# Performance work log

Hardware: AMD Instinct MI355X
Metric: run time of the kernel (lower is better)

## Reference

```python
import jax, jax.numpy as jnp
import numpy as np

N, E, D_IN, D_H, D_OUT = 100000, 1600000, 128, 128, 16


def setup_inputs() -> dict:
    key = jax.random.key(0)
    k_x, k_e, k_w1, k_w2 = jax.random.split(key, 4)
    x = jax.random.normal(k_x, (N, D_IN), dtype=jnp.float32)
    edge_index = jax.random.randint(k_e, (2, E), 0, N, dtype=jnp.int64)
    # glorot-ish init for the two GCNConv weight matrices
    W1 = jax.random.normal(k_w1, (D_IN, D_H), dtype=jnp.float32) * (1.0 / np.sqrt(D_IN))
    b1 = jnp.zeros((D_H,), dtype=jnp.float32)
    W2 = jax.random.normal(k_w2, (D_H, D_OUT), dtype=jnp.float32) * (1.0 / np.sqrt(D_H))
    b2 = jnp.zeros((D_OUT,), dtype=jnp.float32)
    return {"x": x, "edge_index": edge_index, "W1": W1, "b1": b1, "W2": W2, "b2": b2}


def _gcn_conv(x, src, dst, norm, W, b, n):
    # linear transform, gather from source nodes, normalize, scatter-add to targets
    h = x @ W                                   # [N, d_out]
    msg = h[src] * norm[:, None]                # [E+N, d_out]
    return jax.ops.segment_sum(msg, dst, num_segments=n) + b


def reference(x, edge_index, W1, b1, W2, b2):
    n = x.shape[0]
    # GCNConv default: add self-loops, symmetric normalization D^-1/2 A D^-1/2
    loops = jnp.arange(n, dtype=edge_index.dtype)
    src = jnp.concatenate([edge_index[0], loops])
    dst = jnp.concatenate([edge_index[1], loops])
    deg = jax.ops.segment_sum(jnp.ones_like(dst, dtype=x.dtype), dst, num_segments=n)
    dinv = jnp.where(deg > 0, jax.lax.rsqrt(deg), 0.0)
    norm = dinv[src] * dinv[dst]                # [E+N]

    h = _gcn_conv(x, src, dst, norm, W1, b1, n)
    h = jax.nn.relu(h)
    # dropout is identity in eval mode (reference uses eval / deterministic path)
    out = _gcn_conv(h, src, dst, norm, W2, b2, n)
    return out
```

## Files before the change

### kernel.cpp

```cpp
#include <hip/hip_runtime.h>

typedef unsigned int uint;
typedef __attribute__((ext_vector_type(8))) short bf16x8;
typedef __attribute__((ext_vector_type(4))) float f32x4;

#define D_IN 128
#define D_H  128
#define D_OUT 16
#define NPC 512
#define NPCSH 9
#define CLDS 224
#define P1 256
#define XL_STRIDE 68
#define WT_STRIDE 68

static __device__ __forceinline__ float bflo(uint u) { return __uint_as_float(u << 16); }
static __device__ __forceinline__ float bfhi(uint u) { return __uint_as_float(u & 0xFFFF0000u); }
static __device__ __forceinline__ uint f2bf(float f) {
    uint b = __float_as_uint(f);
    return (b + 0x7FFFu + ((b >> 16) & 1u)) >> 16;
}
static __device__ __forceinline__ uint pk(float a, float b) {
    return f2bf(a) | (f2bf(b) << 16);
}


__global__ __launch_bounds__(256) void k_p1hist(const int* __restrict__ dst, int E, int N, int C,
                                                int chunk, int* __restrict__ hist1) {
    __shared__ int h[CLDS];
    int t = threadIdx.x, b = blockIdx.x;
    for (int i = t; i < C; i += 256) h[i] = 0;
    __syncthreads();
    int e0 = b * chunk, e1 = min(e0 + chunk, E);
    for (int e = e0 + t; e < e1; e += 256) {
        int d = dst[e];
        d = max(0, min(d, N - 1));
        atomicAdd(&h[d >> NPCSH], 1);
    }
    __syncthreads();
    for (int i = t; i < C; i += 256) hist1[(size_t)i * P1 + b] = h[i];
}

__global__ __launch_bounds__(1024) void k_p1scan(int* __restrict__ hist1, int C,
                                                 int* __restrict__ cbase) {
    __shared__ int col[CLDS];
    __shared__ int sdata[1024];
    int t = threadIdx.x;
    int w = t >> 6, lane = t & 63;
    for (int i = w; i < C; i += 16) {
        int4 v = ((const int4*)hist1)[i * 64 + lane];
        int s = v.x + v.y + v.z + v.w;
        int inc = s;
        for (int off = 1; off < 64; off <<= 1) {
            int o = __shfl_up(inc, off);
            if (lane >= off) inc += o;
        }
        int excl = inc - s;
        int4 p;
        p.x = excl;
        p.y = excl + v.x;
        p.z = excl + v.x + v.y;
        p.w = excl + v.x + v.y + v.z;
        ((int4*)hist1)[i * 64 + lane] = p;
        if (lane == 63) col[i] = inc;
    }
    __syncthreads();
    int v = (t < C) ? col[t] : 0;
    sdata[t] = v;
    __syncthreads();
    for (int off = 1; off < 1024; off <<= 1) {
        int x = (t >= off) ? sdata[t - off] : 0;
        __syncthreads();
        sdata[t] += x;
        __syncthreads();
    }
    int pos = sdata[t] - v;
    if (t < C) cbase[t] = pos;
    if (t == 1023) cbase[C] = sdata[1023];
    if (t < C) col[t] = pos;
    __syncthreads();
    for (int i = w; i < C; i += 16) {
        int base = col[i];
        int4 p = ((int4*)hist1)[i * 64 + lane];
        p.x += base; p.y += base; p.z += base; p.w += base;
        ((int4*)hist1)[i * 64 + lane] = p;
    }
}

__global__ __launch_bounds__(256) void k_p1fill(const int* __restrict__ src,
                                                const int* __restrict__ dst, int E, int N, int C,
                                                int chunk, const int* __restrict__ hist1,
                                                uint* __restrict__ binned1) {
    __shared__ int cur[CLDS];
    int t = threadIdx.x, b = blockIdx.x;
    for (int i = t; i < C; i += 256) cur[i] = hist1[(size_t)i * P1 + b];
    __syncthreads();
    int e0 = b * chunk, e1 = min(e0 + chunk, E);
    for (int e = e0 + t; e < e1; e += 256) {
        int d = dst[e];
        d = max(0, min(d, N - 1));
        int s = src[e];
        s = max(0, min(s, N - 1));
        int p = atomicAdd(&cur[d >> NPCSH], 1);
        binned1[p] = ((uint)(d & (NPC - 1)) << 17) | (uint)s;
    }
}

__global__ __launch_bounds__(256) void k_p2(const uint* __restrict__ binned1,
                                            const int* __restrict__ cbase, int N,
                                            int* __restrict__ ssrc, int* __restrict__ rowptr,
                                            int* __restrict__ deg, float* __restrict__ dinv) {
    __shared__ int ncnt[NPC], nbase_[NPC];
    __shared__ int sdata[256];
    int c = blockIdx.x, t = threadIdx.x;
    int start = cbase[c], end = cbase[c + 1];
    for (int i = t; i < NPC; i += 256) ncnt[i] = 0;
    __syncthreads();
    for (int j = start + t; j < end; j += 256) atomicAdd(&ncnt[binned1[j] >> 17], 1);
    __syncthreads();
    int v0 = ncnt[2 * t], v1 = ncnt[2 * t + 1];
    int s = v0 + v1;
    sdata[t] = s;
    __syncthreads();
    for (int off = 1; off < 256; off <<= 1) {
        int xv = (t >= off) ? sdata[t - off] : 0;
        __syncthreads();
        sdata[t] += xv;
        __syncthreads();
    }
    int pre = sdata[t] - s;
    nbase_[2 * t] = start + pre;
    nbase_[2 * t + 1] = start + pre + v0;
    __syncthreads();
    for (int i = t; i < NPC; i += 256) {
        int node = c * NPC + i;
        if (node < N) {
            deg[node] = ncnt[i];
            rowptr[node] = nbase_[i];
            dinv[node] = rsqrtf((float)ncnt[i] + 1.0f);
        }
    }
    __syncthreads();
    for (int i = t; i < NPC; i += 256) ncnt[i] = nbase_[i];
    __syncthreads();
    for (int j = start + t; j < end; j += 256) {
        uint pe = binned1[j];
        int p = atomicAdd(&ncnt[pe >> 17], 1);
        ssrc[p] = (int)(pe & 0x1FFFFu);
    }
}


__global__ __launch_bounds__(256) void k_packW1(const float* __restrict__ W1,
                                                uint* __restrict__ W1p) {
    int t = blockIdx.x * 256 + threadIdx.x;
    if (t >= 64 * 128) return;
    int k2 = t >> 7, f = t & 127;
    float w0 = W1[(size_t)(2 * k2) * 128 + f];
    float w1 = W1[(size_t)(2 * k2 + 1) * 128 + f];
    W1p[t] = pk(w0, w1);
}


__global__ __launch_bounds__(256) void k_gemm1(const uint* __restrict__ W1p,
                                               const float* __restrict__ x,
                                               const float* __restrict__ dinv, int N,
                                               uint* __restrict__ hs_b, int ntiles) {
    __shared__ uint Wt[128 * WT_STRIDE];
    __shared__ uint xl[64 * XL_STRIDE];
    int t = threadIdx.x;
    for (int p = t; p < 64 * 128; p += 256) {
        int k2 = p >> 7, f = p & 127;
        Wt[f * WT_STRIDE + k2] = W1p[p];
    }
    int w = t >> 6, lane = t & 63;
    int q = lane >> 4, m = lane & 15;
    const float4* x4 = (const float4*)x;
    for (int tile = blockIdx.x; tile < ntiles; tile += gridDim.x) {
        int row0 = tile * 64;
        __syncthreads();
        for (int p = t; p < 64 * 32; p += 256) {
            int r = p >> 5, c2 = p & 31;
            int gr = row0 + r;
            float4 v = (gr < N) ? x4[(size_t)gr * 32 + c2] : make_float4(0.f, 0.f, 0.f, 0.f);
            *(uint2*)&xl[r * XL_STRIDE + 2 * c2] = make_uint2(pk(v.x, v.y), pk(v.z, v.w));
        }
        __syncthreads();
        bf16x8 afr[4][4];
#pragma unroll
        for (int rt = 0; rt < 4; rt++)
#pragma unroll
            for (int kc = 0; kc < 4; kc++)
                afr[rt][kc] = *(const bf16x8*)&xl[(rt * 16 + m) * XL_STRIDE + kc * 16 + q * 4];
        f32x4 acc[2][4];
#pragma unroll
        for (int c = 0; c < 2; c++)
#pragma unroll
            for (int rt = 0; rt < 4; rt++) acc[c][rt] = (f32x4){0.f, 0.f, 0.f, 0.f};
#pragma unroll
        for (int c = 0; c < 2; c++) {
            int f = w * 32 + c * 16 + m;
#pragma unroll
            for (int kc = 0; kc < 4; kc++) {
                bf16x8 bfr = *(const bf16x8*)&Wt[f * WT_STRIDE + kc * 16 + q * 4];
#pragma unroll
                for (int rt = 0; rt < 4; rt++)
                    acc[c][rt] = __builtin_amdgcn_mfma_f32_16x16x32_bf16(afr[rt][kc], bfr,
                                                                         acc[c][rt], 0, 0, 0);
            }
        }
        __syncthreads();
        uint* outl = xl;
#pragma unroll
        for (int rt = 0; rt < 4; rt++) {
            int gb = row0 + rt * 16 + q * 4;
            float4 dv;
            if (gb + 3 < N) {
                dv = *(const float4*)&dinv[gb];
            } else {
                dv.x = (gb < N) ? dinv[gb] : 0.f;
                dv.y = (gb + 1 < N) ? dinv[gb + 1] : 0.f;
                dv.z = (gb + 2 < N) ? dinv[gb + 2] : 0.f;
                dv.w = (gb + 3 < N) ? dinv[gb + 3] : 0.f;
            }
            float dr[4] = {dv.x, dv.y, dv.z, dv.w};
#pragma unroll
            for (int c = 0; c < 2; c++) {
                f32x4 a = acc[c][rt];
#pragma unroll
                for (int r = 0; r < 4; r++) {
                    float v = a[r] * dr[r];
                    float vn = __shfl_xor(v, 1);
                    if (!(lane & 1)) {
                        int row = rt * 16 + q * 4 + r;
                        int cp = (w * 32 + c * 16 + m) >> 1;
                        outl[row * 65 + cp] = pk(v, vn);
                    }
                }
            }
        }
        __syncthreads();
        for (int p = t; p < 64 * 64; p += 256) {
            int r = p >> 6, cc = p & 63;
            int gr = row0 + r;
            if (gr < N) hs_b[(size_t)gr * 64 + cc] = outl[r * 65 + cc];
        }
    }
}


__global__ __launch_bounds__(256) void k_agg1(const uint* __restrict__ hs_b,
                                              const int* __restrict__ rowptr,
                                              const int* __restrict__ deg,
                                              const int* __restrict__ ssrc,
                                              const float* __restrict__ dinv,
                                              const float2* __restrict__ b1, int N,
                                              uint* __restrict__ rh_b) {
    int w = threadIdx.x >> 6, lane = threadIdx.x & 63;
    int d = blockIdx.x * 4 + w;
    if (d >= N) return;
    int start = rowptr[d], cnt = deg[d];
    uint sv = hs_b[(size_t)d * 64 + lane];
    float a0 = bflo(sv), a1 = bfhi(sv);
    int base = 0;
    while (base < cnt) {
        int nb = min(cnt - base, 64);
        int idxv = (lane < nb) ? ssrc[start + base + lane] : 0;
        int j = 0;
        for (; j + 16 <= nb; j += 16) {
            uint u[16];
#pragma unroll
            for (int q = 0; q < 16; q++) {
                int i = __shfl(idxv, j + q);
                u[q] = hs_b[(size_t)i * 64 + lane];
            }
#pragma unroll
            for (int q = 0; q < 16; q++) {
                a0 += bflo(u[q]);
                a1 += bfhi(u[q]);
            }
        }
        for (; j + 4 <= nb; j += 4) {
            uint u[4];
#pragma unroll
            for (int q = 0; q < 4; q++) {
                int i = __shfl(idxv, j + q);
                u[q] = hs_b[(size_t)i * 64 + lane];
            }
#pragma unroll
            for (int q = 0; q < 4; q++) {
                a0 += bflo(u[q]);
                a1 += bfhi(u[q]);
            }
        }
        for (; j < nb; j++) {
            int i = __shfl(idxv, j);
            uint u = hs_b[(size_t)i * 64 + lane];
            a0 += bflo(u);
            a1 += bfhi(u);
        }
        base += nb;
    }
    float sc = dinv[d];
    float2 bb = b1[lane];
    rh_b[(size_t)d * 64 + lane] =
        pk(fmaxf(fmaf(a0, sc, bb.x), 0.f), fmaxf(fmaf(a1, sc, bb.y), 0.f));
}


__global__ __launch_bounds__(256) void k_gemm2(const uint* __restrict__ rh_b,
                                               const float* __restrict__ W2,
                                               const float* __restrict__ dinv, int N,
                                               uint* __restrict__ h2_b) {
    __shared__ float Wl[D_H * D_OUT];
    int t = threadIdx.x;
    for (int i = t; i < D_H * D_OUT; i += 256) Wl[i] = W2[i];
    __syncthreads();
    int r = blockIdx.x * 256 + t;
    if (r >= N) return;
    const uint* xrow = rh_b + (size_t)r * 64;
    float acc[16];
#pragma unroll
    for (int f = 0; f < 16; f++) acc[f] = 0.f;
    for (int c = 0; c < 16; c++) {
        uint4 xv = *(const uint4*)(xrow + c * 4);
        uint xs[4] = {xv.x, xv.y, xv.z, xv.w};
#pragma unroll
        for (int u = 0; u < 4; u++) {
            int k = c * 8 + u * 2;
            float x0 = bflo(xs[u]), x1 = bfhi(xs[u]);
            const float* w0 = &Wl[k * 16];
            const float* w1 = &Wl[(k + 1) * 16];
#pragma unroll
            for (int f = 0; f < 16; f++) acc[f] = fmaf(x0, w0[f], acc[f]);
#pragma unroll
            for (int f = 0; f < 16; f++) acc[f] = fmaf(x1, w1[f], acc[f]);
        }
    }
    float sc = dinv[r];
    uint o[8];
#pragma unroll
    for (int q = 0; q < 8; q++) o[q] = pk(acc[2 * q] * sc, acc[2 * q + 1] * sc);
    *(uint4*)&h2_b[(size_t)r * 8] = make_uint4(o[0], o[1], o[2], o[3]);
    *(uint4*)&h2_b[(size_t)r * 8 + 4] = make_uint4(o[4], o[5], o[6], o[7]);
}


__global__ __launch_bounds__(256) void k_agg2(const uint* __restrict__ h2_b,
                                              const int* __restrict__ rowptr,
                                              const int* __restrict__ deg,
                                              const int* __restrict__ ssrc,
                                              const float* __restrict__ dinv,
                                              const float* __restrict__ b2, int N,
                                              float2* __restrict__ out) {
    int w = threadIdx.x >> 6, lane = threadIdx.x & 63;
    int d = blockIdx.x * 4 + w;
    if (d >= N) return;
    int slot = lane >> 3, jp = lane & 7;
    int start = rowptr[d], cnt = deg[d];
    float a0 = 0.f, a1 = 0.f;
    if (slot == 0) {
        uint sv = h2_b[(size_t)d * 8 + jp];
        a0 = bflo(sv);
        a1 = bfhi(sv);
    }
    int base = 0;
    while (base < cnt) {
        int nb = min(cnt - base, 64);
        int idxv = (lane < nb) ? ssrc[start + base + lane] : 0;
        int ngroups = (nb + 7) >> 3;
        for (int g = 0; g < ngroups; g++) {
            int j = g * 8 + slot;
            int i = __shfl(idxv, j);
            if (j < nb) {
                uint hv = h2_b[(size_t)i * 8 + jp];
                a0 += bflo(hv);
                a1 += bfhi(hv);
            }
        }
        base += nb;
    }
    a0 += __shfl_xor(a0, 8);
    a1 += __shfl_xor(a1, 8);
    a0 += __shfl_xor(a0, 16);
    a1 += __shfl_xor(a1, 16);
    a0 += __shfl_xor(a0, 32);
    a1 += __shfl_xor(a1, 32);
    if (slot == 0) {
        float di = dinv[d];
        out[(size_t)d * 8 + jp] =
            make_float2(fmaf(a0, di, b2[2 * jp]), fmaf(a1, di, b2[2 * jp + 1]));
    }
}


extern "C" void kernel_launch(void* const* d_in, const int* in_sizes, int n_in,
                              void* d_out, int out_size, void* d_ws, size_t ws_size,
                              hipStream_t stream) {
    const float* x  = (const float*)d_in[0];
    const int*   ei = (const int*)d_in[1];
    const float* W1 = (const float*)d_in[2];
    const float* b1 = (const float*)d_in[3];
    const float* W2 = (const float*)d_in[4];
    const float* b2 = (const float*)d_in[5];
    int N = in_sizes[0] / D_IN;
    int E = in_sizes[1] / 2;
    const int* src = ei;
    const int* dst = ei + E;
    int C = (N + NPC - 1) / NPC;
    int chunk = (E + P1 - 1) / P1;
    int ntiles = (N + 63) / 64;

    char* ws = (char*)d_ws;
    size_t off = 0;
    auto alloc = [&](size_t bytes) -> char* {
        char* p = ws + off;
        off = (off + bytes + 255) & ~(size_t)255;
        return p;
    };
    int*   hist1   = (int*)alloc((size_t)P1 * C * 4);
    int*   cbase   = (int*)alloc((size_t)(C + 1) * 4);
    uint*  binned1 = (uint*)alloc((size_t)E * 4);
    int*   ssrc    = (int*)alloc((size_t)E * 4);
    int*   rowptr  = (int*)alloc((size_t)N * 4);
    int*   deg     = (int*)alloc((size_t)N * 4);
    float* dinv    = (float*)alloc((size_t)N * 4);
    uint*  W1p     = (uint*)alloc((size_t)64 * 128 * 4);
    uint*  hs_b    = (uint*)alloc((size_t)N * 64 * 4);
    uint*  rh_b    = (uint*)alloc((size_t)N * 64 * 4);
    uint*  h2_b    = hs_b;

    k_packW1<<<32, 256, 0, stream>>>(W1, W1p);
    k_p1hist<<<P1, 256, 0, stream>>>(dst, E, N, C, chunk, hist1);
    k_p1scan<<<1, 1024, 0, stream>>>(hist1, C, cbase);
    k_p1fill<<<P1, 256, 0, stream>>>(src, dst, E, N, C, chunk, hist1, binned1);
    k_p2<<<C, 256, 0, stream>>>(binned1, cbase, N, ssrc, rowptr, deg, dinv);
    int g1 = min(768, ntiles);
    k_gemm1<<<g1, 256, 0, stream>>>(W1p, x, dinv, N, hs_b, ntiles);
    k_agg1<<<(N + 3) / 4, 256, 0, stream>>>(hs_b, rowptr, deg, ssrc, dinv,
                                            (const float2*)b1, N, rh_b);
    k_gemm2<<<(N + 255) / 256, 256, 0, stream>>>(rh_b, W2, dinv, N, h2_b);
    k_agg2<<<(N + 3) / 4, 256, 0, stream>>>(h2_b, rowptr, deg, ssrc, dinv, b2, N,
                                            (float2*)d_out);
}
```

Baseline: 295.1 us.

## Fuse CSR build with GEMM1, move source dinv scaling into aggregation

The W1 packing is folded into extra blocks of the histogram kernel, and the per-cluster CSR finalize (k_p2) now runs as extra blocks of the GEMM1 launch. GEMM1 no longer depends on dinv, so the two run concurrently. To allow this, the source-side dinv scaling moves from GEMM1's epilogue into agg1, which gathers dinv per neighbor and uses FMAs. agg2 also gets a specialized path for small-degree nodes that issues four independent loads per lane. The cost is two fewer launches and overlap of the CSR and GEMM work, traded for an extra random dinv gather per edge in agg1 and larger shared-memory use in the fused CSR blocks.

```diff
diff --git a/kernel.cpp b/kernel.cpp
--- a/kernel.cpp
+++ b/kernel.cpp
@@ -26,9 +26,19 @@
 
 
 __global__ __launch_bounds__(256) void k_p1hist(const int* __restrict__ dst, int E, int N, int C,
-                                                int chunk, int* __restrict__ hist1) {
+                                                int chunk, int* __restrict__ hist1,
+                                                const float* __restrict__ W1,
+                                                uint* __restrict__ W1p) {
     __shared__ int h[CLDS];
     int t = threadIdx.x, b = blockIdx.x;
+    if (b >= P1) {
+        int p = (b - P1) * 256 + t;
+        int k2 = p >> 7, f = p & 127;
+        float w0 = W1[(size_t)(2 * k2) * 128 + f];
+        float w1 = W1[(size_t)(2 * k2 + 1) * 128 + f];
+        W1p[p] = pk(w0, w1);
+        return;
+    }
     for (int i = t; i < C; i += 256) h[i] = 0;
     __syncthreads();
     int e0 = b * chunk, e1 = min(e0 + chunk, E);
@@ -106,69 +116,62 @@
     }
 }
 
-__global__ __launch_bounds__(256) void k_p2(const uint* __restrict__ binned1,
-                                            const int* __restrict__ cbase, int N,
-                                            int* __restrict__ ssrc, int* __restrict__ rowptr,
-                                            int* __restrict__ deg, float* __restrict__ dinv) {
-    __shared__ int ncnt[NPC], nbase_[NPC];
-    __shared__ int sdata[256];
-    int c = blockIdx.x, t = threadIdx.x;
-    int start = cbase[c], end = cbase[c + 1];
-    for (int i = t; i < NPC; i += 256) ncnt[i] = 0;
-    __syncthreads();
-    for (int j = start + t; j < end; j += 256) atomicAdd(&ncnt[binned1[j] >> 17], 1);
-    __syncthreads();
-    int v0 = ncnt[2 * t], v1 = ncnt[2 * t + 1];
-    int s = v0 + v1;
-    sdata[t] = s;
-    __syncthreads();
-    for (int off = 1; off < 256; off <<= 1) {
-        int xv = (t >= off) ? sdata[t - off] : 0;
-        __syncthreads();
-        sdata[t] += xv;
-        __syncthreads();
-    }
-    int pre = sdata[t] - s;
-    nbase_[2 * t] = start + pre;
-    nbase_[2 * t + 1] = start + pre + v0;
-    __syncthreads();
-    for (int i = t; i < NPC; i += 256) {
-        int node = c * NPC + i;
-        if (node < N) {
-            deg[node] = ncnt[i];
-            rowptr[node] = nbase_[i];
-            dinv[node] = rsqrtf((float)ncnt[i] + 1.0f);
-        }
-    }
-    __syncthreads();
-    for (int i = t; i < NPC; i += 256) ncnt[i] = nbase_[i];
-    __syncthreads();
-    for (int j = start + t; j < end; j += 256) {
-        uint pe = binned1[j];
-        int p = atomicAdd(&ncnt[pe >> 17], 1);
-        ssrc[p] = (int)(pe & 0x1FFFFu);
-    }
-}
-
-
-__global__ __launch_bounds__(256) void k_packW1(const float* __restrict__ W1,
-                                                uint* __restrict__ W1p) {
-    int t = blockIdx.x * 256 + threadIdx.x;
-    if (t >= 64 * 128) return;
-    int k2 = t >> 7, f = t & 127;
-    float w0 = W1[(size_t)(2 * k2) * 128 + f];
-    float w1 = W1[(size_t)(2 * k2 + 1) * 128 + f];
-    W1p[t] = pk(w0, w1);
-}
-
-
-__global__ __launch_bounds__(256) void k_gemm1(const uint* __restrict__ W1p,
-                                               const float* __restrict__ x,
-                                               const float* __restrict__ dinv, int N,
-                                               uint* __restrict__ hs_b, int ntiles) {
-    __shared__ uint Wt[128 * WT_STRIDE];
-    __shared__ uint xl[64 * XL_STRIDE];
+
+__global__ __launch_bounds__(256) void k_p2gemm1(const uint* __restrict__ binned1,
+                                                 const int* __restrict__ cbase, int N, int C,
+                                                 int* __restrict__ ssrc, int* __restrict__ rowptr,
+                                                 int* __restrict__ deg, float* __restrict__ dinv,
+                                                 const uint* __restrict__ W1p,
+                                                 const float* __restrict__ x,
+                                                 uint* __restrict__ hs_b, int ntiles) {
+    __shared__ uint smem[128 * WT_STRIDE + 64 * XL_STRIDE];
     int t = threadIdx.x;
+    if ((int)blockIdx.x < C) {
+        int* ncnt = (int*)smem;
+        int* nbase_ = ncnt + NPC;
+        int* sdata = nbase_ + NPC;
+        int c = blockIdx.x;
+        int start = cbase[c], end = cbase[c + 1];
+        for (int i = t; i < NPC; i += 256) ncnt[i] = 0;
+        __syncthreads();
+        for (int j = start + t; j < end; j += 256) atomicAdd(&ncnt[binned1[j] >> 17], 1);
+        __syncthreads();
+        int v0 = ncnt[2 * t], v1 = ncnt[2 * t + 1];
+        int s = v0 + v1;
+        sdata[t] = s;
+        __syncthreads();
+        for (int off = 1; off < 256; off <<= 1) {
+            int xv = (t >= off) ? sdata[t - off] : 0;
+            __syncthreads();
+            sdata[t] += xv;
+            __syncthreads();
+        }
+        int pre = sdata[t] - s;
+        nbase_[2 * t] = start + pre;
+        nbase_[2 * t + 1] = start + pre + v0;
+        __syncthreads();
+        for (int i = t; i < NPC; i += 256) {
+            int node = c * NPC + i;
+            if (node < N) {
+                deg[node] = ncnt[i];
+                rowptr[node] = nbase_[i];
+                dinv[node] = rsqrtf((float)ncnt[i] + 1.0f);
+            }
+        }
+        __syncthreads();
+        for (int i = t; i < NPC; i += 256) ncnt[i] = nbase_[i];
+        __syncthreads();
+        for (int j = start + t; j < end; j += 256) {
+            uint pe = binned1[j];
+            int p = atomicAdd(&ncnt[pe >> 17], 1);
+            ssrc[p] = (int)(pe & 0x1FFFFu);
+        }
+        return;
+    }
+    uint* Wt = smem;
+    uint* xl = smem + 128 * WT_STRIDE;
+    int role = blockIdx.x - C;
+    int nroles = gridDim.x - C;
     for (int p = t; p < 64 * 128; p += 256) {
         int k2 = p >> 7, f = p & 127;
         Wt[f * WT_STRIDE + k2] = W1p[p];
@@ -176,7 +179,7 @@
     int w = t >> 6, lane = t & 63;
     int q = lane >> 4, m = lane & 15;
     const float4* x4 = (const float4*)x;
-    for (int tile = blockIdx.x; tile < ntiles; tile += gridDim.x) {
+    for (int tile = role; tile < ntiles; tile += nroles) {
         int row0 = tile * 64;
         __syncthreads();
         for (int p = t; p < 64 * 32; p += 256) {
@@ -213,23 +216,12 @@
         uint* outl = xl;
 #pragma unroll
         for (int rt = 0; rt < 4; rt++) {
-            int gb = row0 + rt * 16 + q * 4;
-            float4 dv;
-            if (gb + 3 < N) {
-                dv = *(const float4*)&dinv[gb];
-            } else {
-                dv.x = (gb < N) ? dinv[gb] : 0.f;
-                dv.y = (gb + 1 < N) ? dinv[gb + 1] : 0.f;
-                dv.z = (gb + 2 < N) ? dinv[gb + 2] : 0.f;
-                dv.w = (gb + 3 < N) ? dinv[gb + 3] : 0.f;
-            }
-            float dr[4] = {dv.x, dv.y, dv.z, dv.w};
 #pragma unroll
             for (int c = 0; c < 2; c++) {
                 f32x4 a = acc[c][rt];
 #pragma unroll
                 for (int r = 0; r < 4; r++) {
-                    float v = a[r] * dr[r];
+                    float v = a[r];
                     float vn = __shfl_xor(v, 1);
                     if (!(lane & 1)) {
                         int row = rt * 16 + q * 4 + r;
@@ -260,48 +252,54 @@
     int d = blockIdx.x * 4 + w;
     if (d >= N) return;
     int start = rowptr[d], cnt = deg[d];
+    float sc = dinv[d];
     uint sv = hs_b[(size_t)d * 64 + lane];
-    float a0 = bflo(sv), a1 = bfhi(sv);
+    float a0 = bflo(sv) * sc, a1 = bfhi(sv) * sc;
     int base = 0;
     while (base < cnt) {
         int nb = min(cnt - base, 64);
         int idxv = (lane < nb) ? ssrc[start + base + lane] : 0;
+        float dvv = dinv[idxv];
         int j = 0;
         for (; j + 16 <= nb; j += 16) {
             uint u[16];
+            float dv[16];
 #pragma unroll
             for (int q = 0; q < 16; q++) {
                 int i = __shfl(idxv, j + q);
+                dv[q] = __shfl(dvv, j + q);
                 u[q] = hs_b[(size_t)i * 64 + lane];
             }
 #pragma unroll
             for (int q = 0; q < 16; q++) {
-                a0 += bflo(u[q]);
-                a1 += bfhi(u[q]);
+                a0 = fmaf(bflo(u[q]), dv[q], a0);
+                a1 = fmaf(bfhi(u[q]), dv[q], a1);
             }
         }
         for (; j + 4 <= nb; j += 4) {
             uint u[4];
+            float dv[4];
 #pragma unroll
             for (int q = 0; q < 4; q++) {
                 int i = __shfl(idxv, j + q);
+                dv[q] = __shfl(dvv, j + q);
                 u[q] = hs_b[(size_t)i * 64 + lane];
             }
 #pragma unroll
             for (int q = 0; q < 4; q++) {
-                a0 += bflo(u[q]);
-                a1 += bfhi(u[q]);
+                a0 = fmaf(bflo(u[q]), dv[q], a0);
+                a1 = fmaf(bfhi(u[q]), dv[q], a1);
             }
         }
         for (; j < nb; j++) {
             int i = __shfl(idxv, j);
+            float dv = __shfl(dvv, j);
             uint u = hs_b[(size_t)i * 64 + lane];
-            a0 += bflo(u);
-            a1 += bfhi(u);
+            a0 = fmaf(bflo(u), dv, a0);
+            a1 = fmaf(bfhi(u), dv, a1);
         }
         base += nb;
     }
-    float sc = dinv[d];
     float2 bb = b1[lane];
     rh_b[(size_t)d * 64 + lane] =
         pk(fmaxf(fmaf(a0, sc, bb.x), 0.f), fmaxf(fmaf(a1, sc, bb.y), 0.f));
@@ -368,14 +366,27 @@
     while (base < cnt) {
         int nb = min(cnt - base, 64);
         int idxv = (lane < nb) ? ssrc[start + base + lane] : 0;
-        int ngroups = (nb + 7) >> 3;
-        for (int g = 0; g < ngroups; g++) {
-            int j = g * 8 + slot;
-            int i = __shfl(idxv, j);
-            if (j < nb) {
-                uint hv = h2_b[(size_t)i * 8 + jp];
-                a0 += bflo(hv);
-                a1 += bfhi(hv);
+        int ng = (nb + 7) >> 3;
+        if (ng <= 4) {
+            int i0 = __shfl(idxv, slot);
+            int i1 = __shfl(idxv, 8 + slot);
+            int i2 = __shfl(idxv, 16 + slot);
+            int i3 = __shfl(idxv, 24 + slot);
+            uint u0 = (slot < nb) ? h2_b[(size_t)i0 * 8 + jp] : 0u;
+            uint u1 = (8 + slot < nb) ? h2_b[(size_t)i1 * 8 + jp] : 0u;
+            uint u2 = (16 + slot < nb) ? h2_b[(size_t)i2 * 8 + jp] : 0u;
+            uint u3 = (24 + slot < nb) ? h2_b[(size_t)i3 * 8 + jp] : 0u;
+            a0 += bflo(u0) + bflo(u1) + bflo(u2) + bflo(u3);
+            a1 += bfhi(u0) + bfhi(u1) + bfhi(u2) + bfhi(u3);
+        } else {
+            for (int g = 0; g < ng; g++) {
+                int j = g * 8 + slot;
+                int i = __shfl(idxv, j);
+                if (j < nb) {
+                    uint hv = h2_b[(size_t)i * 8 + jp];
+                    a0 += bflo(hv);
+                    a1 += bfhi(hv);
+                }
             }
         }
         base += nb;
@@ -430,13 +441,12 @@
     uint*  rh_b    = (uint*)alloc((size_t)N * 64 * 4);
     uint*  h2_b    = hs_b;
 
-    k_packW1<<<32, 256, 0, stream>>>(W1, W1p);
-    k_p1hist<<<P1, 256, 0, stream>>>(dst, E, N, C, chunk, hist1);
+    k_p1hist<<<P1 + 32, 256, 0, stream>>>(dst, E, N, C, chunk, hist1, W1, W1p);
     k_p1scan<<<1, 1024, 0, stream>>>(hist1, C, cbase);
     k_p1fill<<<P1, 256, 0, stream>>>(src, dst, E, N, C, chunk, hist1, binned1);
-    k_p2<<<C, 256, 0, stream>>>(binned1, cbase, N, ssrc, rowptr, deg, dinv);
     int g1 = min(768, ntiles);
-    k_gemm1<<<g1, 256, 0, stream>>>(W1p, x, dinv, N, hs_b, ntiles);
+    k_p2gemm1<<<C + g1, 256, 0, stream>>>(binned1, cbase, N, C, ssrc, rowptr, deg, dinv,
+                                          W1p, x, hs_b, ntiles);
     k_agg1<<<(N + 3) / 4, 256, 0, stream>>>(hs_b, rowptr, deg, ssrc, dinv,
                                             (const float2*)b1, N, rh_b);
     k_gemm2<<<(N + 255) / 256, 256, 0, stream>>>(rh_b, W2, dinv, N, h2_b);
```

Measured after the change: 278.5 us. -5.6%, faster.
